# Optimization experiments

Hardware: AMD Instinct MI355X
Metric: run time of the kernel (lower is better)

The kernel has to match this reference:

```python
import jax, jax.numpy as jnp
import numpy as np

B, H, S, E = 16384, 1024, 256, 8


def setup_inputs() -> dict:
    key = jax.random.key(0)
    ks = jax.random.split(key, 10)
    s = 0.02  # init scale
    return {
        "x": jax.random.normal(ks[0], (B, H), jnp.float32),
        "user_embedding": jax.random.normal(ks[1], (B, H), jnp.float32),
        "sw1": jax.random.normal(ks[2], (H, S), jnp.float32) * s,
        "sb1": jnp.zeros((S,), jnp.float32),
        "sw2": jax.random.normal(ks[3], (S, E), jnp.float32) * s,
        "sb2": jnp.zeros((E,), jnp.float32),
        "ew1": jax.random.normal(ks[4], (E, H, H), jnp.float32) * s,
        "eb1": jnp.zeros((E, H), jnp.float32),
        "ew2": jax.random.normal(ks[5], (E, H, H), jnp.float32) * s,
        "eb2": jnp.zeros((E, H), jnp.float32),
        "uw1": jax.random.normal(ks[6], (H, H), jnp.float32) * s,
        "ub1": jnp.zeros((H,), jnp.float32),
        "uw2": jax.random.normal(ks[7], (H, H), jnp.float32) * s,
        "ub2": jnp.zeros((H,), jnp.float32),
    }


def reference(x, user_embedding, sw1, sb1, sw2, sb2, ew1, eb1, ew2, eb2, uw1, ub1, uw2, ub2):
    # Router: 2-layer MLP on user_embedding -> softmax -> top-1 route.
    logits = jax.nn.relu(user_embedding @ sw1 + sb1) @ sw2 + sb2  # [B, E]
    route_prob = jax.nn.softmax(logits, axis=-1)
    routes = jnp.argmax(route_prob, axis=-1)  # [B] int

    # Experts: compute all experts densely (E small, fixed), then gather per token.
    # Dropout layers are inference no-ops.
    h = jax.nn.relu(jnp.einsum('bh,ehd->ebd', x, ew1) + eb1[:, None, :])   # [E, B, H]
    eo = jnp.einsum('ebd,edh->ebh', h, ew2) + eb2[:, None, :]               # [E, B, H]
    expert_out = jnp.take_along_axis(eo, routes[None, :, None], axis=0)[0]  # [B, H]

    # Shared user-expert FFN applied to every token.
    uexpert_out = jax.nn.relu(x @ uw1 + ub1) @ uw2 + ub2  # [B, H]

    return expert_out + uexpert_out
```

## Files before the change

### kernel.cpp

```cpp
#include <hip/hip_runtime.h>
#include <stdint.h>

#define NTOK 16384
#define HD   1024
#define SD   256
#define NE   8

typedef short bf16x8 __attribute__((ext_vector_type(8)));
typedef _Float16 f16x8 __attribute__((ext_vector_type(8)));
typedef float f32x4 __attribute__((ext_vector_type(4)));
typedef unsigned short u16;
typedef unsigned short u16x8 __attribute__((ext_vector_type(8)));

__device__ __forceinline__ u16 f2bf(float f) {
  union { float f; unsigned u; } v; v.f = f;
  return (u16)((v.u + 0x7fffu + ((v.u >> 16) & 1u)) >> 16);
}

__device__ __forceinline__ void gload16(const void* g, void* l) {
  __builtin_amdgcn_global_load_lds((const __attribute__((address_space(1))) void*)g,
                                   (__attribute__((address_space(3))) void*)l,
                                   16, 0, 0);
}



__global__ __launch_bounds__(256) void prep_kernel(
    const float* __restrict__ ue, _Float16* __restrict__ aP,
    const float* __restrict__ sw1, _Float16* __restrict__ bP) {
  const int bid = blockIdx.x;
  const int tid = threadIdx.x;
  if (bid < 8192) {
    const int t = bid * 256 + tid;
    const int p = t >> 7;
    const int h = (t & 127) << 3;
    const float* s = ue + ((size_t)p << 10) + h;
    const float4 a = *(const float4*)s;
    const float4 b = *(const float4*)(s + 4);
    float v[8] = {a.x, a.y, a.z, a.w, b.x, b.y, b.z, b.w};
    f16x8 hi, lo;
#pragma unroll
    for (int j = 0; j < 8; ++j) {
      const _Float16 h16 = (_Float16)v[j];
      hi[j] = h16;
      lo[j] = (_Float16)(v[j] - (float)h16);
    }
    _Float16* d = aP + ((size_t)p << 11) + h;
    *(f16x8*)d = hi;
    *(f16x8*)(d + 1024) = lo;
    return;
  }
  __shared__ float tb[64][65];
  const int b = bid - 8192;
  const int c0 = (b & 3) << 6;
  const int r0 = (b >> 2) << 6;
  {
    const int lr = tid >> 2, q = (tid & 3) << 4;
    const float* s = sw1 + (size_t)(r0 + lr) * SD + c0 + q;
#pragma unroll
    for (int j = 0; j < 16; j += 4) {
      const float4 v = *(const float4*)(s + j);
      tb[lr][q + j] = v.x; tb[lr][q + j + 1] = v.y;
      tb[lr][q + j + 2] = v.z; tb[lr][q + j + 3] = v.w;
    }
  }
  __syncthreads();
  const int lc = tid >> 2, rq = (tid & 3) << 4;
  f16x8 hi0, hi1, lo0, lo1;
#pragma unroll
  for (int j = 0; j < 8; ++j) {
    const float v0 = tb[rq + j][lc];
    const _Float16 h0 = (_Float16)v0;
    hi0[j] = h0; lo0[j] = (_Float16)(v0 - (float)h0);
    const float v1 = tb[rq + 8 + j][lc];
    const _Float16 h1 = (_Float16)v1;
    hi1[j] = h1; lo1[j] = (_Float16)(v1 - (float)h1);
  }
  _Float16* d = bP + (size_t)(c0 + lc) * 3072 + r0 + rq;
  *(f16x8*)d = hi0;           *(f16x8*)(d + 8) = hi1;
  *(f16x8*)(d + 1024) = lo0;  *(f16x8*)(d + 1032) = lo1;
  *(f16x8*)(d + 2048) = hi0;  *(f16x8*)(d + 2056) = hi1;
}

__global__ __launch_bounds__(256) void rtconv_kernel(
    const _Float16* __restrict__ aP, const _Float16* __restrict__ bP,
    const float* __restrict__ sb1, float* __restrict__ hidden,
    const float* __restrict__ ew1, const float* __restrict__ ew2,
    const float* __restrict__ uw1, const float* __restrict__ uw2,
    u16* __restrict__ ew1t, u16* __restrict__ ew2t,
    u16* __restrict__ uw1t, u16* __restrict__ uw2t) {
  __shared__ char smem[24576];
  const int bid = blockIdx.x;
  const int tid = threadIdx.x;

  if (bid < 512) {
    _Float16 (*sA)[128 * 32] = (_Float16(*)[128 * 32])smem;
    _Float16 (*sB)[64 * 32]  = (_Float16(*)[64 * 32])(smem + 16384);

    const int L = (bid & 7) * 64 + (bid >> 3);
    const int jt = L & 3;
    const int row0 = (L >> 2) << 7;

    const int lane = tid & 63, wave = tid >> 6;
    const int wr = (wave >> 1) << 6, wc = (wave & 1) << 5;
    const int smrow = tid >> 2, skoff = (((tid & 3) ^ ((tid >> 3) & 3)) << 3);
    const _Float16* ar0 = aP + ((size_t)(row0 + smrow) << 11) + skoff;
    const _Float16* ar1 = aP + ((size_t)(row0 + smrow + 64) << 11) + skoff;
    const _Float16* br  = bP + (size_t)((jt << 6) + smrow) * 3072 + skoff;
    const int ldsoff = wave << 10;

    f32x4 acc[4][2];
#pragma unroll
    for (int i = 0; i < 4; ++i)
#pragma unroll
      for (int j = 0; j < 2; ++j) acc[i][j] = (f32x4){0.f, 0.f, 0.f, 0.f};

    gload16(ar0, (char*)sA[0] + ldsoff);
    gload16(ar1, (char*)sA[0] + 4096 + ldsoff);
    gload16(br,  (char*)sB[0] + ldsoff);

    const int sl = (((lane >> 4) ^ ((lane >> 1) & 3)) << 3);
    const int afrag = (wr + (lane & 15)) * 32 + sl;
    const int bfrag = (wc + (lane & 15)) * 32 + sl;

#pragma unroll
    for (int ks = 0; ks < 96; ++ks) {
      const int buf = ks & 1;
      __syncthreads();
      if (ks + 1 < 96) {
        const int k1 = ks + 1;
        const int pa = (k1 < 64) ? ((k1 & 31) << 5) : (1024 + ((k1 - 64) << 5));
        gload16(ar0 + pa, (char*)sA[buf ^ 1] + ldsoff);
        gload16(ar1 + pa, (char*)sA[buf ^ 1] + 4096 + ldsoff);
        gload16(br + (k1 << 5), (char*)sB[buf ^ 1] + ldsoff);
      }
      f16x8 av[4], bv[2];
#pragma unroll
      for (int f = 0; f < 4; ++f) av[f] = *(const f16x8*)&sA[buf][afrag + f * 512];
#pragma unroll
      for (int f = 0; f < 2; ++f) bv[f] = *(const f16x8*)&sB[buf][bfrag + f * 512];
#pragma unroll
      for (int i = 0; i < 4; ++i)
#pragma unroll
        for (int j = 0; j < 2; ++j)
          acc[i][j] = __builtin_amdgcn_mfma_f32_16x16x32_f16(av[i], bv[j], acc[i][j], 0, 0, 0);
    }

    const int lc = lane & 15, lr4 = (lane >> 4) << 2;
#pragma unroll
    for (int j = 0; j < 2; ++j) {
      const int c = (jt << 6) + wc + (j << 4) + lc;
      const float bias = sb1[c];
#pragma unroll
      for (int i = 0; i < 4; ++i) {
        const int rl = wr + (i << 4) + lr4;
#pragma unroll
        for (int q = 0; q < 4; ++q)
          hidden[((size_t)(row0 + rl + q) << 8) + c] = fmaxf(acc[i][j][q] + bias, 0.f);
      }
    }
    return;
  }

  float (*tb)[65] = (float(*)[65])smem;
  const int c = bid - 512;
  const int m = c >> 8;
  const int t2 = c & 255;
  const int c0 = (t2 & 15) << 6;
  const int r0 = (t2 >> 4) << 6;
  const size_t msz = (size_t)HD * HD;
  const float* src; u16* dst;
  if (m < 8)       { src = ew1 + (size_t)m * msz;       dst = ew1t + (size_t)m * msz; }
  else if (m < 16) { src = ew2 + (size_t)(m - 8) * msz; dst = ew2t + (size_t)(m - 8) * msz; }
  else if (m == 16){ src = uw1;                          dst = uw1t; }
  else             { src = uw2;                          dst = uw2t; }
  {
    const int lr = tid >> 2, q = (tid & 3) << 4;
    const float* s = src + (size_t)(r0 + lr) * HD + c0 + q;
#pragma unroll
    for (int j = 0; j < 16; j += 4) {
      const float4 v = *(const float4*)(s + j);
      tb[lr][q + j] = v.x; tb[lr][q + j + 1] = v.y;
      tb[lr][q + j + 2] = v.z; tb[lr][q + j + 3] = v.w;
    }
  }
  __syncthreads();
  {
    const int lc = tid >> 2, rq = (tid & 3) << 4;
    u16x8 o0, o1;
#pragma unroll
    for (int j = 0; j < 8; ++j) o0[j] = f2bf(tb[rq + j][lc]);
#pragma unroll
    for (int j = 0; j < 8; ++j) o1[j] = f2bf(tb[rq + 8 + j][lc]);
    u16* d = dst + (size_t)(c0 + lc) * HD + r0 + rq;
    *(u16x8*)d = o0;
    *(u16x8*)(d + 8) = o1;
  }
}

__global__ __launch_bounds__(256) void logits_kernel(
    const float* __restrict__ hidden, const float* __restrict__ sw2,
    const float* __restrict__ sb2, int* __restrict__ routes, int* meta) {
  __shared__ float logl[32][8];
  __shared__ int lhist[NE];
  const int tid = threadIdx.x;
  if (tid < NE) lhist[tid] = 0;
  const int tok0 = blockIdx.x << 7;
  const int tl = tid >> 3, e2 = tid & 7;
  __syncthreads();
#pragma unroll 1
  for (int g4 = 0; g4 < 4; ++g4) {
    const float* hp = hidden + ((size_t)(tok0 + (g4 << 5) + tl) << 8);
    float a0 = 0.f, a1 = 0.f, a2 = 0.f, a3 = 0.f;
    for (int q = 0; q < SD; q += 8) {
      const float4 h0 = *(const float4*)&hp[q];
      const float4 h1 = *(const float4*)&hp[q + 4];
      a0 = fmaf(h0.x, sw2[((q + 0) << 3) + e2], a0);
      a1 = fmaf(h0.y, sw2[((q + 1) << 3) + e2], a1);
      a2 = fmaf(h0.z, sw2[((q + 2) << 3) + e2], a2);
      a3 = fmaf(h0.w, sw2[((q + 3) << 3) + e2], a3);
      a0 = fmaf(h1.x, sw2[((q + 4) << 3) + e2], a0);
      a1 = fmaf(h1.y, sw2[((q + 5) << 3) + e2], a1);
      a2 = fmaf(h1.z, sw2[((q + 6) << 3) + e2], a2);
      a3 = fmaf(h1.w, sw2[((q + 7) << 3) + e2], a3);
    }
    logl[tl][e2] = (a0 + a1) + (a2 + a3) + sb2[e2];
    __syncthreads();
    if (tid < 32) {
      float best = logl[tid][0]; int be = 0;
#pragma unroll
      for (int e = 1; e < 8; ++e) {
        const float v = logl[tid][e];
        if (v > best) { best = v; be = e; }
      }
      routes[tok0 + (g4 << 5) + tid] = be;
      atomicAdd(&lhist[be], 1);
    }
    __syncthreads();
  }
  if (tid < NE) atomicAdd(&meta[tid], lhist[tid]);
  __syncthreads();
  if (tid == 0) {
    __threadfence();
    const int done = atomicAdd(&meta[26], 1);
    if (done == (int)gridDim.x - 1) {
      int cnt[NE];
#pragma unroll
      for (int e = 0; e < NE; ++e) cnt[e] = atomicAdd(&meta[e], 0);
      int off = 0;
      for (int e = 0; e < NE; ++e) { meta[16 + e] = off; off += cnt[e]; }
      meta[24] = off;
      int nt = 0;
      for (int e = 0; e < NE; ++e) {
        const int s = meta[16 + e], en = meta[16 + e + 1];
        for (int r0 = s; r0 < en; r0 += 128) {
          meta[32 + nt] = e; meta[192 + nt] = r0; meta[352 + nt] = en; ++nt;
        }
      }
      meta[25] = nt;
      __threadfence();
    }
  }
}

__global__ __launch_bounds__(256) void perm_kernel(
    const int* __restrict__ routes, int* meta, int* __restrict__ perm) {
  __shared__ int lcnt[NE], lbase[NE], lcur[NE];
  const int tid = threadIdx.x;
  if (tid < NE) { lcnt[tid] = 0; lcur[tid] = 0; }
  __syncthreads();
  const int b = blockIdx.x * 256 + tid;
  const int r = routes[b];
  atomicAdd(&lcnt[r], 1);
  __syncthreads();
  if (tid < NE)
    lbase[tid] = meta[16 + tid] + atomicAdd(&meta[8 + tid], lcnt[tid]);
  __syncthreads();
  const int rank = atomicAdd(&lcur[r], 1);
  perm[lbase[r] + rank] = b;
}

__global__ __launch_bounds__(256) void gatherx_kernel(
    const float* __restrict__ x, const int* __restrict__ perm, u16* __restrict__ xg) {
  const int t = blockIdx.x * 256 + threadIdx.x;
  const int p = t >> 7;
  const int j = (t & 127) << 3;
  const int tok = perm[p];
  const float* s = &x[((size_t)tok << 10) + j];
  const float4 a = *(const float4*)s;
  const float4 b = *(const float4*)(s + 4);
  u16x8 o;
  o[0] = f2bf(a.x); o[1] = f2bf(a.y); o[2] = f2bf(a.z); o[3] = f2bf(a.w);
  o[4] = f2bf(b.x); o[5] = f2bf(b.y); o[6] = f2bf(b.z); o[7] = f2bf(b.w);
  *(u16x8*)&xg[((size_t)p << 10) + j] = o;
}

__global__ __launch_bounds__(256) void gemm1_kernel(
    const u16* __restrict__ xg, const u16* __restrict__ ew1t,
    const u16* __restrict__ uw1t, const float* __restrict__ eb1,
    const float* __restrict__ ub1, const int* __restrict__ meta,
    u16* __restrict__ hid) {
  const int nt = meta[25];
  const int pb = blockIdx.x;
  const int L = (pb & 7) * 270 + (pb >> 3);
  const int mt = L >> 4;
  const int jt = L & 15;
  if (mt >= nt) return;
  const int e = meta[32 + mt], row0 = meta[192 + mt], gend = meta[352 + mt];
  const u16* wbase = (jt < 8)
      ? ew1t + ((size_t)e << 20) + ((size_t)(jt << 7) << 10)
      : uw1t + ((size_t)((jt - 8) << 7) << 10);

  __shared__ u16 smem[16384];
  u16 (*sA)[4096] = (u16(*)[4096])smem;
  u16 (*sB)[4096] = (u16(*)[4096])(smem + 8192);

  const int tid = threadIdx.x;
  const int lane = tid & 63;
  const int wave = tid >> 6;
  const int wr = (wave >> 1) << 6;
  const int wc = (wave & 1) << 6;

  const int smrow = tid >> 2;
  const int skoff = (((tid & 3) ^ ((tid >> 3) & 3)) << 3);
  const u16* ap0 = xg + (((size_t)(row0 + smrow)) << 10) + skoff;
  const u16* ap1 = xg + (((size_t)(row0 + smrow + 64)) << 10) + skoff;
  const u16* bp0 = wbase + (((size_t)smrow) << 10) + skoff;
  const u16* bp1 = wbase + (((size_t)(smrow + 64)) << 10) + skoff;
  const int ldsoff = wave << 10;

  f32x4 acc[4][4];
#pragma unroll
  for (int i = 0; i < 4; ++i)
#pragma unroll
    for (int j = 0; j < 4; ++j) acc[i][j] = (f32x4){0.f, 0.f, 0.f, 0.f};

  gload16(ap0, (char*)sA[0] + ldsoff);
  gload16(ap1, (char*)sA[0] + 4096 + ldsoff);
  gload16(bp0, (char*)sB[0] + ldsoff);
  gload16(bp1, (char*)sB[0] + 4096 + ldsoff);

  const int sl = (((lane >> 4) ^ ((lane >> 1) & 3)) << 3);
  const int afrag = (wr + (lane & 15)) * 32 + sl;
  const int bfrag = (wc + (lane & 15)) * 32 + sl;

#pragma unroll
  for (int ks = 0; ks < 32; ++ks) {
    const int buf = ks & 1;
    __syncthreads();
    if (ks + 1 < 32) {
      const int k1 = (ks + 1) << 5;
      gload16(ap0 + k1, (char*)sA[buf ^ 1] + ldsoff);
      gload16(ap1 + k1, (char*)sA[buf ^ 1] + 4096 + ldsoff);
      gload16(bp0 + k1, (char*)sB[buf ^ 1] + ldsoff);
      gload16(bp1 + k1, (char*)sB[buf ^ 1] + 4096 + ldsoff);
    }
    bf16x8 av[4], bv[4];
#pragma unroll
    for (int f = 0; f < 4; ++f) {
      av[f] = *(const bf16x8*)&sA[buf][afrag + f * 512];
      bv[f] = *(const bf16x8*)&sB[buf][bfrag + f * 512];
    }
#pragma unroll
    for (int i = 0; i < 4; ++i)
#pragma unroll
      for (int j = 0; j < 4; ++j)
        acc[i][j] = __builtin_amdgcn_mfma_f32_16x16x32_bf16(av[i], bv[j], acc[i][j], 0, 0, 0);
  }

  __syncthreads();
  {
    const int lc = lane & 15;
    const int lr4 = (lane >> 4) << 2;
#pragma unroll
    for (int j = 0; j < 4; ++j) {
      const int c = wc + (j << 4) + lc;
      const int gc = (jt << 7) + c;
      const float bias = (gc < 1024) ? eb1[(e << 10) + gc] : ub1[gc - 1024];
#pragma unroll
      for (int i = 0; i < 4; ++i) {
        const int rl = wr + (i << 4) + lr4;
#pragma unroll
        for (int q = 0; q < 4; ++q)
          smem[(rl + q) * 128 + c] = f2bf(fmaxf(acc[i][j][q] + bias, 0.f));
      }
    }
  }
  __syncthreads();
  {
    const int l16 = lane & 15, rg = lane >> 4;
#pragma unroll
    for (int it = 0; it < 8; ++it) {
      const int lr = (wave << 5) + (it << 2) + rg;
      const int p = row0 + lr;
      const u16x8 v = *(const u16x8*)&smem[lr * 128 + (l16 << 3)];
      if (p < gend)
        *(u16x8*)&hid[((size_t)p << 11) + (jt << 7) + (l16 << 3)] = v;
    }
  }
}

__global__ __launch_bounds__(256) void gemm2_kernel(
    const u16* __restrict__ hid, const u16* __restrict__ ew2t,
    const u16* __restrict__ uw2t, const float* __restrict__ eb2,
    const float* __restrict__ ub2, const int* __restrict__ meta,
    const int* __restrict__ perm, float* __restrict__ out) {
  const int nt = meta[25];
  const int pb = blockIdx.x;
  const int L = (pb & 7) * 135 + (pb >> 3);
  const int mt = L >> 3;
  const int jt = L & 7;
  if (mt >= nt) return;
  const int e = meta[32 + mt], row0 = meta[192 + mt], gend = meta[352 + mt];
  const int n0 = jt << 7;

  __shared__ u16 smem[16384];
  u16 (*sA)[4096] = (u16(*)[4096])smem;
  u16 (*sB)[4096] = (u16(*)[4096])(smem + 8192);
  float* smemf = (float*)smem;

  const int tid = threadIdx.x;
  const int lane = tid & 63;
  const int wave = tid >> 6;
  const int wr = (wave >> 1) << 6;
  const int wc = (wave & 1) << 6;

  const int smrow = tid >> 2;
  const int skoff = (((tid & 3) ^ ((tid >> 3) & 3)) << 3);
  const u16* ap0 = hid + (((size_t)(row0 + smrow)) << 11) + skoff;
  const u16* ap1 = hid + (((size_t)(row0 + smrow + 64)) << 11) + skoff;
  const u16* ebase = ew2t + ((size_t)e << 20);
  const size_t brow0 = (((size_t)(n0 + smrow)) << 10) + skoff;
  const size_t brow1 = (((size_t)(n0 + smrow + 64)) << 10) + skoff;
  const int ldsoff = wave << 10;

  f32x4 acc[4][4];
#pragma unroll
  for (int i = 0; i < 4; ++i)
#pragma unroll
    for (int j = 0; j < 4; ++j) acc[i][j] = (f32x4){0.f, 0.f, 0.f, 0.f};

  gload16(ap0, (char*)sA[0] + ldsoff);
  gload16(ap1, (char*)sA[0] + 4096 + ldsoff);
  gload16(ebase + brow0, (char*)sB[0] + ldsoff);
  gload16(ebase + brow1, (char*)sB[0] + 4096 + ldsoff);

  const int sl = (((lane >> 4) ^ ((lane >> 1) & 3)) << 3);
  const int afrag = (wr + (lane & 15)) * 32 + sl;
  const int bfrag = (wc + (lane & 15)) * 32 + sl;

#pragma unroll
  for (int ks = 0; ks < 64; ++ks) {
    const int buf = ks & 1;
    __syncthreads();
    if (ks + 1 < 64) {
      const int k1 = (ks + 1) << 5;
      const u16* bb = (k1 < 1024) ? ebase : uw2t;
      const int kk = k1 & 1023;
      gload16(ap0 + k1, (char*)sA[buf ^ 1] + ldsoff);
      gload16(ap1 + k1, (char*)sA[buf ^ 1] + 4096 + ldsoff);
      gload16(bb + brow0 + kk, (char*)sB[buf ^ 1] + ldsoff);
      gload16(bb + brow1 + kk, (char*)sB[buf ^ 1] + 4096 + ldsoff);
    }
    bf16x8 av[4], bv[4];
#pragma unroll
    for (int f = 0; f < 4; ++f) {
      av[f] = *(const bf16x8*)&sA[buf][afrag + f * 512];
      bv[f] = *(const bf16x8*)&sB[buf][bfrag + f * 512];
    }
#pragma unroll
    for (int i = 0; i < 4; ++i)
#pragma unroll
      for (int j = 0; j < 4; ++j)
        acc[i][j] = __builtin_amdgcn_mfma_f32_16x16x32_bf16(av[i], bv[j], acc[i][j], 0, 0, 0);
  }

  const int lc = lane & 15;
  const int lr4 = (lane >> 4) << 2;
  float b2v[4];
#pragma unroll
  for (int j = 0; j < 4; ++j) {
    const int c = n0 + wc + (j << 4) + lc;
    b2v[j] = eb2[(e << 10) + c] + ub2[c];
  }
  __syncthreads();
#pragma unroll
  for (int pass = 0; pass < 2; ++pass) {
    if ((wave >> 1) == pass) {
#pragma unroll
      for (int j = 0; j < 4; ++j) {
        const int c = wc + (j << 4) + lc;
#pragma unroll
        for (int i = 0; i < 4; ++i) {
          const int lrl = (i << 4) + lr4;
#pragma unroll
          for (int q = 0; q < 4; ++q)
            smemf[(lrl + q) * 128 + c] = acc[i][j][q] + b2v[j];
        }
      }
    }
    __syncthreads();
#pragma unroll
    for (int it = 0; it < 8; ++it) {
      const int lrl = (it << 3) + (wave << 1) + (lane >> 5);
      const int p = row0 + (pass << 6) + lrl;
      const float4 v = *(const float4*)&smemf[lrl * 128 + ((lane & 31) << 2)];
      if (p < gend)
        *(float4*)&out[((size_t)perm[p] << 10) + n0 + ((lane & 31) << 2)] = v;
    }
    __syncthreads();
  }
}

extern "C" void kernel_launch(void* const* d_in, const int* in_sizes, int n_in,
                              void* d_out, int out_size, void* d_ws, size_t ws_size,
                              hipStream_t stream) {
  const float* x   = (const float*)d_in[0];
  const float* ue  = (const float*)d_in[1];
  const float* sw1 = (const float*)d_in[2];
  const float* sb1 = (const float*)d_in[3];
  const float* sw2 = (const float*)d_in[4];
  const float* sb2 = (const float*)d_in[5];
  const float* ew1 = (const float*)d_in[6];
  const float* eb1 = (const float*)d_in[7];
  const float* ew2 = (const float*)d_in[8];
  const float* eb2 = (const float*)d_in[9];
  const float* uw1 = (const float*)d_in[10];
  const float* ub1 = (const float*)d_in[11];
  const float* uw2 = (const float*)d_in[12];
  const float* ub2 = (const float*)d_in[13];
  float* out = (float*)d_out;

  char* w = (char*)d_ws;
  int* meta = (int*)w;    w += 4096;
  int* routes = (int*)w;  w += NTOK * 4;
  int* perm = (int*)w;    w += NTOK * 4;
  char* region = w;
  u16* xg   = (u16*)region;
  u16* ew1t = (u16*)(region + 33816576ull);
  u16* ew2t = (u16*)(region + 33816576ull + 16777216ull);
  u16* uw1t = (u16*)(region + 33816576ull + 2 * 16777216ull);
  u16* uw2t = (u16*)(region + 33816576ull + 2 * 16777216ull + 2097152ull);
  u16* hid  = (u16*)(region + 33816576ull + 2 * 16777216ull + 2 * 2097152ull);
  const size_t region_sz = 33816576ull + 2 * 16777216ull + 2 * 2097152ull + 67633152ull;
  _Float16* aP     = (_Float16*)(region + 33816576ull + 2 * 16777216ull + 2 * 2097152ull);
  float* hidden32  = (float*)region;
  _Float16* bP     = (_Float16*)(region + 16777216ull);
  if (135168ull + region_sz > ws_size) return;

  hipMemsetAsync(meta, 0, 4096, stream);
  prep_kernel<<<8256, 256, 0, stream>>>(ue, aP, sw1, bP);
  rtconv_kernel<<<5120, 256, 0, stream>>>(aP, bP, sb1, hidden32,
                                          ew1, ew2, uw1, uw2,
                                          ew1t, ew2t, uw1t, uw2t);
  logits_kernel<<<NTOK / 128, 256, 0, stream>>>(hidden32, sw2, sb2, routes, meta);
  perm_kernel<<<NTOK / 256, 256, 0, stream>>>(routes, meta, perm);
  gatherx_kernel<<<(NTOK * 128) / 256, 256, 0, stream>>>(x, perm, xg);
  gemm1_kernel<<<2160, 256, 0, stream>>>(xg, ew1t, uw1t, eb1, ub1, meta, hid);
  gemm2_kernel<<<1080, 256, 0, stream>>>(hid, ew2t, uw2t, eb2, ub2, meta, perm, out);
}
```

Measured before the change: 339.8 us.

## Fold x bf16 conversion into earlier kernels and gather rows inside gemm1

Drops the separate gatherx kernel. x is now converted to bf16 in original token order: the tail rows are handled by extra blocks in rtconv_kernel, and the remaining rows by extra blocks in the perm kernel. gemm1 then reads A rows through the perm index instead of from a pre-permuted buffer. This removes one launch and lets the conversion traffic overlap with other work, at the cost of indirect row addresses in gemm1 and careful aliasing of the shared workspace region.

```diff
diff --git a/kernel.cpp b/kernel.cpp
--- a/kernel.cpp
+++ b/kernel.cpp
@@ -21,6 +21,21 @@
   __builtin_amdgcn_global_load_lds((const __attribute__((address_space(1))) void*)g,
                                    (__attribute__((address_space(3))) void*)l,
                                    16, 0, 0);
+}
+
+__device__ __forceinline__ void xcvt_rows(const float* __restrict__ x,
+                                          u16* __restrict__ xg,
+                                          int row_base, int blk, int tid) {
+  const int t = blk * 256 + tid;
+  const int p = row_base + (t >> 7);
+  const int j = (t & 127) << 3;
+  const float* s = &x[((size_t)p << 10) + j];
+  const float4 a = *(const float4*)s;
+  const float4 b = *(const float4*)(s + 4);
+  u16x8 o;
+  o[0] = f2bf(a.x); o[1] = f2bf(a.y); o[2] = f2bf(a.z); o[3] = f2bf(a.w);
+  o[4] = f2bf(b.x); o[5] = f2bf(b.y); o[6] = f2bf(b.z); o[7] = f2bf(b.w);
+  *(u16x8*)&xg[((size_t)p << 10) + j] = o;
 }
 
 
@@ -88,11 +103,16 @@
     const float* __restrict__ ew1, const float* __restrict__ ew2,
     const float* __restrict__ uw1, const float* __restrict__ uw2,
     u16* __restrict__ ew1t, u16* __restrict__ ew2t,
-    u16* __restrict__ uw1t, u16* __restrict__ uw2t) {
+    u16* __restrict__ uw1t, u16* __restrict__ uw2t,
+    const float* __restrict__ x, u16* __restrict__ xg) {
   __shared__ char smem[24576];
   const int bid = blockIdx.x;
   const int tid = threadIdx.x;
 
+  if (bid >= 5120) {
+    xcvt_rows(x, xg, 8960, bid - 5120, tid);
+    return;
+  }
   if (bid < 512) {
     _Float16 (*sA)[128 * 32] = (_Float16(*)[128 * 32])smem;
     _Float16 (*sB)[64 * 32]  = (_Float16(*)[64 * 32])(smem + 16384);
@@ -263,13 +283,19 @@
   }
 }
 
-__global__ __launch_bounds__(256) void perm_kernel(
-    const int* __restrict__ routes, int* meta, int* __restrict__ perm) {
+__global__ __launch_bounds__(256) void permx_kernel(
+    const int* __restrict__ routes, int* meta, int* __restrict__ perm,
+    const float* __restrict__ x, u16* __restrict__ xg) {
+  const int bid = blockIdx.x;
+  const int tid = threadIdx.x;
+  if (bid >= 64) {
+    xcvt_rows(x, xg, 0, bid - 64, tid);
+    return;
+  }
   __shared__ int lcnt[NE], lbase[NE], lcur[NE];
-  const int tid = threadIdx.x;
   if (tid < NE) { lcnt[tid] = 0; lcur[tid] = 0; }
   __syncthreads();
-  const int b = blockIdx.x * 256 + tid;
+  const int b = bid * 256 + tid;
   const int r = routes[b];
   atomicAdd(&lcnt[r], 1);
   __syncthreads();
@@ -278,28 +304,13 @@
   __syncthreads();
   const int rank = atomicAdd(&lcur[r], 1);
   perm[lbase[r] + rank] = b;
-}
-
-__global__ __launch_bounds__(256) void gatherx_kernel(
-    const float* __restrict__ x, const int* __restrict__ perm, u16* __restrict__ xg) {
-  const int t = blockIdx.x * 256 + threadIdx.x;
-  const int p = t >> 7;
-  const int j = (t & 127) << 3;
-  const int tok = perm[p];
-  const float* s = &x[((size_t)tok << 10) + j];
-  const float4 a = *(const float4*)s;
-  const float4 b = *(const float4*)(s + 4);
-  u16x8 o;
-  o[0] = f2bf(a.x); o[1] = f2bf(a.y); o[2] = f2bf(a.z); o[3] = f2bf(a.w);
-  o[4] = f2bf(b.x); o[5] = f2bf(b.y); o[6] = f2bf(b.z); o[7] = f2bf(b.w);
-  *(u16x8*)&xg[((size_t)p << 10) + j] = o;
 }
 
 __global__ __launch_bounds__(256) void gemm1_kernel(
     const u16* __restrict__ xg, const u16* __restrict__ ew1t,
     const u16* __restrict__ uw1t, const float* __restrict__ eb1,
     const float* __restrict__ ub1, const int* __restrict__ meta,
-    u16* __restrict__ hid) {
+    const int* __restrict__ perm, u16* __restrict__ hid) {
   const int nt = meta[25];
   const int pb = blockIdx.x;
   const int L = (pb & 7) * 270 + (pb >> 3);
@@ -323,8 +334,10 @@
 
   const int smrow = tid >> 2;
   const int skoff = (((tid & 3) ^ ((tid >> 3) & 3)) << 3);
-  const u16* ap0 = xg + (((size_t)(row0 + smrow)) << 10) + skoff;
-  const u16* ap1 = xg + (((size_t)(row0 + smrow + 64)) << 10) + skoff;
+  int rr0 = row0 + smrow;       if (rr0 > NTOK - 1) rr0 = NTOK - 1;
+  int rr1 = row0 + smrow + 64;  if (rr1 > NTOK - 1) rr1 = NTOK - 1;
+  const u16* ap0 = xg + (((size_t)perm[rr0]) << 10) + skoff;
+  const u16* ap1 = xg + (((size_t)perm[rr1]) << 10) + skoff;
   const u16* bp0 = wbase + (((size_t)smrow) << 10) + skoff;
   const u16* bp1 = wbase + (((size_t)(smrow + 64)) << 10) + skoff;
   const int ldsoff = wave << 10;
@@ -550,12 +563,11 @@
 
   hipMemsetAsync(meta, 0, 4096, stream);
   prep_kernel<<<8256, 256, 0, stream>>>(ue, aP, sw1, bP);
-  rtconv_kernel<<<5120, 256, 0, stream>>>(aP, bP, sb1, hidden32,
+  rtconv_kernel<<<8832, 256, 0, stream>>>(aP, bP, sb1, hidden32,
                                           ew1, ew2, uw1, uw2,
-                                          ew1t, ew2t, uw1t, uw2t);
+                                          ew1t, ew2t, uw1t, uw2t, x, xg);
   logits_kernel<<<NTOK / 128, 256, 0, stream>>>(hidden32, sw2, sb2, routes, meta);
-  perm_kernel<<<NTOK / 256, 256, 0, stream>>>(routes, meta, perm);
-  gatherx_kernel<<<(NTOK * 128) / 256, 256, 0, stream>>>(x, perm, xg);
-  gemm1_kernel<<<2160, 256, 0, stream>>>(xg, ew1t, uw1t, eb1, ub1, meta, hid);
+  permx_kernel<<<64 + 4480, 256, 0, stream>>>(routes, meta, perm, x, xg);
+  gemm1_kernel<<<2160, 256, 0, stream>>>(xg, ew1t, uw1t, eb1, ub1, meta, perm, hid);
   gemm2_kernel<<<1080, 256, 0, stream>>>(hid, ew2t, uw2t, eb2, ub2, meta, perm, out);
 }
```

After: 333.6 us. About the same (-1.8%).
